# Performance work log

Measured on AMD Instinct MI355X. Metric: run time of the kernel, lower is better.

Reference implementation:

```python
import jax, jax.numpy as jnp
import numpy as np

HID = 64        # hid_size
NUM_LAYER = 3
NG = 16         # number of graphs in batch
NPG = 160       # nodes per graph
N = NG * NPG    # 2560 total nodes
DEG = 16
EPG = NPG * DEG # edges per graph
E = NG * EPG    # 40960 total edges
P = NG * NPG * NPG  # 409600 total (i,j) pairs from triu_indices(n, -n)
AV = 64         # atom feature vocab per column (9 columns)
BV = 8          # bond feature vocab per column (3 columns)
EPS = 1e-5


def setup_inputs() -> dict:
    rng = np.random.default_rng(0)
    key = jax.random.key(0)
    ks = jax.random.split(key, 16)

    # categorical node / edge features
    x = jnp.asarray(rng.integers(0, AV, size=(N, 9)), dtype=jnp.int32)
    edge_attr = jnp.asarray(rng.integers(0, BV, size=(E, 3)), dtype=jnp.int32)

    # within-graph random edges (sorted order not required for the math here)
    src_l = rng.integers(0, NPG, size=(NG, EPG))
    dst_l = rng.integers(0, NPG, size=(NG, EPG))
    gid = np.repeat(np.arange(NG), EPG)
    # flat position of edge (u,v) of graph g inside the concatenated all-pairs list
    epos = jnp.asarray(gid * NPG * NPG + src_l.reshape(-1) * NPG + dst_l.reshape(-1),
                       dtype=jnp.int32)

    # idx = concat([triu_indices(n, -n) + ptr[g]]) -> all pairs, row-major per graph
    g = np.arange(NG)[:, None, None]
    i = np.arange(NPG)[None, :, None]
    j = np.arange(NPG)[None, None, :]
    idx0 = jnp.asarray(np.broadcast_to(g * NPG + i, (NG, NPG, NPG)).reshape(-1).astype(np.int32))
    idx1 = jnp.asarray(np.broadcast_to(g * NPG + j, (NG, NPG, NPG)).reshape(-1).astype(np.int32))

    def lin(k, fan_in, fan_out):
        b = 1.0 / np.sqrt(fan_in)
        kw, kb = jax.random.split(k)
        return (jax.random.uniform(kw, (fan_in, fan_out), jnp.float32, -b, b),
                jax.random.uniform(kb, (fan_out,), jnp.float32, -b, b))

    atom_tables = jax.random.normal(ks[0], (9, AV, HID), jnp.float32) * 0.02
    bond_tables = jax.random.normal(ks[1], (3, BV, HID), jnp.float32) * 0.02
    W1, b1 = lin(ks[2], HID, HID)
    W2, b2 = lin(ks[3], HID, HID)
    We, be = lin(ks[4], HID, HID)
    L0_w, L0_b = lin(ks[5], 3 * HID, HID)
    L1_w, L1_b = lin(ks[6], HID, HID)
    L2_w, L2_b = lin(ks[7], HID, 1)
    g0 = jnp.ones((HID,), jnp.float32); beta0 = jnp.zeros((HID,), jnp.float32)
    g1 = jnp.ones((HID,), jnp.float32); beta1 = jnp.zeros((HID,), jnp.float32)

    return dict(atom_tables=atom_tables, bond_tables=bond_tables,
                W1=W1, b1=b1, W2=W2, b2=b2, We=We, be=be,
                L0_w=L0_w, L0_b=L0_b, L1_w=L1_w, L1_b=L1_b, L2_w=L2_w, L2_b=L2_b,
                g0=g0, beta0=beta0, g1=g1, beta1=beta1,
                x=x, edge_attr=edge_attr, idx0=idx0, idx1=idx1, epos=epos)


def _batchnorm(h, gamma, beta):
    mu = jnp.mean(h, axis=0)
    var = jnp.mean(jnp.square(h - mu), axis=0)  # biased var, torch training mode
    return (h - mu) * jax.lax.rsqrt(var + EPS) * gamma + beta


def reference(atom_tables, bond_tables, W1, b1, W2, b2, We, be,
              L0_w, L0_b, L1_w, L1_b, L2_w, L2_b,
              g0, beta0, g1, beta1,
              x, edge_attr, idx0, idx1, epos):
    # AtomEncoder / BondEncoder: sum of per-column embedding lookups
    cols9 = jnp.arange(9)[None, :]
    x_emb = atom_tables[cols9, x].sum(axis=1)          # [N, HID]
    cols3 = jnp.arange(3)[None, :]
    ea_emb = bond_tables[cols3, edge_attr].sum(axis=1)  # [E, HID]

    n1 = (x_emb @ W1 + b1)[idx0]                        # [P, HID]
    n2 = (x_emb @ W2 + b2)[idx1]                        # [P, HID]

    e = ea_emb @ We + be                                # [E, HID]
    # equivalent of SparseTensor.to_dense()[idx0, idx1] without the N^2 dense blowup;
    # duplicate edges sum, missing pairs are zero (matches to_dense semantics)
    e_pairs = jnp.zeros((P, HID), e.dtype).at[epos].add(e)

    emb = jnp.concatenate((n1, n2, e_pairs), axis=-1)   # [P, 3*HID]

    emb = jax.nn.relu(_batchnorm(emb @ L0_w + L0_b, g0, beta0))
    emb = jax.nn.relu(_batchnorm(emb @ L1_w + L1_b, g1, beta1))
    emb = emb @ L2_w + L2_b                             # [P, 1]
    return jnp.squeeze(emb, axis=-1)                    # [P]
```

## Files before the change

kernel.cpp:

```cpp
#include <hip/hip_runtime.h>
#include <hip/hip_bf16.h>

#define HID 64
#define NGr 16
#define NPG 160
#define NN  2560
#define EE  40960
#define PPG 25600
#define PT  409600
#define TT  25600
#define TPG 1600
#define AV  64
#define BV  8
#define EPSB 1e-5f

typedef __attribute__((ext_vector_type(8))) short short8v;
typedef __attribute__((ext_vector_type(4))) float f32x4;

static __device__ __forceinline__ unsigned short bf16_hi(float v) {
    return (unsigned short)(__float_as_uint(v) >> 16);
}
static __device__ __forceinline__ unsigned short bf16_rn(float v) {
    unsigned int u = __float_as_uint(v);
    u += 0x7FFFu + ((u >> 16) & 1u);
    return (unsigned short)(u >> 16);
}
static __device__ __forceinline__ float bf16_val(unsigned short h) {
    return __uint_as_float(((unsigned int)h) << 16);
}

__global__ void k_prep(const float* __restrict__ W1, const float* __restrict__ b1,
                       const float* __restrict__ W2, const float* __restrict__ b2,
                       const float* __restrict__ We, const float* __restrict__ be,
                       const float* __restrict__ L0w, const float* __restrict__ L0b,
                       const float* __restrict__ L1w,
                       float* __restrict__ W1c, float* __restrict__ W2c, float* __restrict__ Wec,
                       float* __restrict__ b1c, float* __restrict__ b2c, float* __restrict__ bec,
                       float* __restrict__ stats,
                       unsigned short* __restrict__ WBhi, unsigned short* __restrict__ WBlo) {
    int blk = blockIdx.x, tid = threadIdx.x;
    if (blk == 3) {
        stats[tid] = 0.f;
        for (int idx = tid; idx < 4096; idx += 256) {
            float w = L1w[idx];
            unsigned short hi = bf16_hi(w);
            float rem = w - bf16_val(hi);
            WBhi[idx] = hi;
            WBlo[idx] = bf16_hi(rem);
        }
        return;
    }
    const float* Wsrc = (blk == 0) ? W1 : (blk == 1) ? W2 : We;
    const float* bsrc = (blk == 0) ? b1 : (blk == 1) ? b2 : be;
    const float* L    = L0w + blk * 64 * 64;
    float* Wdst = (blk == 0) ? W1c : (blk == 1) ? W2c : Wec;
    float* bdst = (blk == 0) ? b1c : (blk == 1) ? b2c : bec;
    for (int idx = tid; idx < 4096; idx += 256) {
        int k = idx >> 6, h = idx & 63;
        float acc = 0.f;
        for (int m = 0; m < 64; ++m) acc = fmaf(Wsrc[k * 64 + m], L[m * 64 + h], acc);
        Wdst[idx] = acc;
    }
    if (tid < 64) {
        int h = tid;
        float acc = (blk == 0) ? L0b[h] : 0.f;
        for (int m = 0; m < 64; ++m) acc = fmaf(bsrc[m], L[m * 64 + h], acc);
        bdst[h] = acc;
    }
}

__global__ void __launch_bounds__(256) k_nodes(const float* __restrict__ atab, const int* __restrict__ x,
                        const float* __restrict__ W1c, const float* __restrict__ W2c,
                        const float* __restrict__ b1c, const float* __restrict__ b2c,
                        float* __restrict__ A, float* __restrict__ Bm) {
    int w = threadIdx.x >> 6, h = threadIdx.x & 63;
    int n = blockIdx.x * 4 + w;
    __shared__ float xe[4][64];
    float v = 0.f;
#pragma unroll
    for (int c = 0; c < 9; ++c) v += atab[c * AV * HID + x[n * 9 + c] * HID + h];
    xe[w][h] = v;
    float a = b1c[h], b = b2c[h];
#pragma unroll
    for (int k = 0; k < 64; ++k) {
        float xk = xe[w][k];
        a = fmaf(xk, W1c[k * 64 + h], a);
        b = fmaf(xk, W2c[k * 64 + h], b);
    }
    A[n * 64 + h] = a;
    Bm[n * 64 + h] = b;
}

__global__ void k_gstats(const float* __restrict__ A, const float* __restrict__ Bm,
                         float* __restrict__ stats) {
    int g = blockIdx.x;
    int h = threadIdx.x & 63, w = threadIdx.x >> 6;
    float sA = 0.f, sA2 = 0.f, sB = 0.f, sB2 = 0.f;
    for (int n = w; n < NPG; n += 4) {
        float a = A[(size_t)(g * NPG + n) * 64 + h];
        float b = Bm[(size_t)(g * NPG + n) * 64 + h];
        sA += a; sA2 = fmaf(a, a, sA2);
        sB += b; sB2 = fmaf(b, b, sB2);
    }
    __shared__ float ls[4][4][64];
    ls[w][0][h] = sA; ls[w][1][h] = sA2; ls[w][2][h] = sB; ls[w][3][h] = sB2;
    __syncthreads();
    if (w == 0) {
        sA  = ls[0][0][h] + ls[1][0][h] + ls[2][0][h] + ls[3][0][h];
        sA2 = ls[0][1][h] + ls[1][1][h] + ls[2][1][h] + ls[3][1][h];
        sB  = ls[0][2][h] + ls[1][2][h] + ls[2][2][h] + ls[3][2][h];
        sB2 = ls[0][3][h] + ls[1][3][h] + ls[2][3][h] + ls[3][3][h];
        atomicAdd(&stats[h], 160.f * (sA + sB));
        atomicAdd(&stats[64 + h], 160.f * (sA2 + sB2) + 2.f * sA * sB);
    }
}

__global__ void __launch_bounds__(256) k_edges(const float* __restrict__ btab, const int* __restrict__ eattr,
                                               const int* __restrict__ epos,
                                               const float* __restrict__ Wec, const float* __restrict__ bec,
                                               float* __restrict__ ewf, float* __restrict__ stats,
                                               int* __restrict__ bcount) {
    int h = threadIdx.x & 63;
    int el = threadIdx.x >> 6;
    __shared__ float ea[4][64];
    float ssum = 0.f;
    for (int base = blockIdx.x * 4; base < EE; base += gridDim.x * 4) {
        int e = base + el;
        float v = 0.f;
#pragma unroll
        for (int c = 0; c < 3; ++c) v += btab[c * BV * HID + eattr[e * 3 + c] * HID + h];
        ea[el][h] = v;
        float ew = bec[h];
#pragma unroll
        for (int k = 0; k < 64; ++k) ew = fmaf(ea[el][k], Wec[k * 64 + h], ew);
        ewf[(size_t)e * 64 + h] = ew;
        ssum += ew;
        if (h == 0) atomicAdd(&bcount[epos[e] >> 4], 1);
    }
    atomicAdd(&stats[h], ssum);
}

__global__ void k_scan(const int* __restrict__ bcount, int* __restrict__ boffs,
                       int* __restrict__ bcursor) {
    __shared__ int part[1024];
    int tid = threadIdx.x;
    int base = tid * (TT / 1024);
    int s = 0;
    for (int q = 0; q < TT / 1024; ++q) s += bcount[base + q];
    part[tid] = s;
    __syncthreads();
    for (int d = 1; d < 1024; d <<= 1) {
        int v = (tid >= d) ? part[tid - d] : 0;
        __syncthreads();
        part[tid] += v;
        __syncthreads();
    }
    int run = part[tid] - s;
    for (int q = 0; q < TT / 1024; ++q) {
        int c = bcount[base + q];
        boffs[base + q] = run;
        bcursor[base + q] = run;
        run += c;
    }
    if (tid == 1023) boffs[TT] = run;
}

__global__ void k_fill(const int* __restrict__ epos, int* __restrict__ bcursor,
                       int* __restrict__ elist) {
    int e = blockIdx.x * 256 + threadIdx.x;
    if (e >= EE) return;
    int p = epos[e];
    int t = p >> 4, jj = p & 15;
    int slot = atomicAdd(&bcursor[t], 1);
    elist[slot] = (e << 4) | jj;
}

__global__ void __launch_bounds__(256) k_scorr(const float* __restrict__ A, const float* __restrict__ Bm,
                                               const float* __restrict__ ewf,
                                               const int* __restrict__ boffs, const int* __restrict__ elist,
                                               float* __restrict__ stats) {
    __shared__ float run[4][16][64];
    int h = threadIdx.x & 63, w = threadIdx.x >> 6;
#pragma unroll
    for (int jj = 0; jj < 16; ++jj) run[w][jj][h] = 0.f;
    float ssacc = 0.f;
    int wave = blockIdx.x * 4 + w;
    int nw = gridDim.x * 4;
    for (int t = wave; t < TT; t += nw) {
        int be = boffs[t], en = boffs[t + 1];
        if (be == en) continue;
        int g = t / TPG;
        int rem = t - g * TPG;
        int i = rem / 10;
        int j0 = (rem - i * 10) << 4;
        float a = A[(size_t)(g * NPG + i) * 64 + h];
        for (int q = be; q < en; ++q) {
            int pk = elist[q];
            int e = pk >> 4, jj = pk & 15;
            float ew = ewf[(size_t)e * 64 + h];
            float base = a + Bm[(size_t)(g * NPG + j0 + jj) * 64 + h];
            float r = run[w][jj][h];
            ssacc += 2.f * (base + r) * ew + ew * ew;
            run[w][jj][h] = r + ew;
        }
        for (int q = be; q < en; ++q) run[w][elist[q] & 15][h] = 0.f;
    }
    atomicAdd(&stats[64 + h], ssacc);
}

__global__ void __launch_bounds__(256) k_main(const unsigned short* __restrict__ WBhi,
                                              const unsigned short* __restrict__ WBlo,
                                              const float* __restrict__ L1b,
                                              const float* __restrict__ g0, const float* __restrict__ beta0,
                                              const float* __restrict__ A, const float* __restrict__ Bm,
                                              const float* __restrict__ ewf,
                                              const int* __restrict__ boffs, const int* __restrict__ elist,
                                              uint2* __restrict__ zpk, float* __restrict__ stats) {
    int lane = threadIdx.x & 63;
    int wid  = blockIdx.x * 4 + (threadIdx.x >> 6);
    int nWaves = gridDim.x * 4;
    int r16 = lane & 15;
    int kg  = lane >> 4;

    const float invP = 1.f / (float)PT;
    float s0a[8], t0a[8], s0b[8], t0b[8];
#pragma unroll
    for (int j = 0; j < 8; ++j) {
        int k = kg * 8 + j;
        float mu = stats[k] * invP;
        float var = stats[64 + k] * invP - mu * mu;
        float inv = rsqrtf(var + EPSB);
        s0a[j] = g0[k] * inv;
        t0a[j] = fmaf(-mu, s0a[j], beta0[k]);
        int k2 = k + 32;
        float mu2 = stats[k2] * invP;
        float var2 = stats[64 + k2] * invP - mu2 * mu2;
        float inv2 = rsqrtf(var2 + EPSB);
        s0b[j] = g0[k2] * inv2;
        t0b[j] = fmaf(-mu2, s0b[j], beta0[k2]);
    }
    short8v Bhi[4][2], Blo[4][2];
#pragma unroll
    for (int ct = 0; ct < 4; ++ct)
#pragma unroll
        for (int ks = 0; ks < 2; ++ks)
#pragma unroll
            for (int j = 0; j < 8; ++j) {
                int k = ks * 32 + kg * 8 + j;
                int idx = k * 64 + ct * 16 + r16;
                Bhi[ct][ks][j] = (short)WBhi[idx];
                Blo[ct][ks][j] = (short)WBlo[idx];
            }
    float biasv[4];
#pragma unroll
    for (int ct = 0; ct < 4; ++ct) biasv[ct] = L1b[ct * 16 + r16];

    float sum[4] = {0.f, 0.f, 0.f, 0.f}, ssum[4] = {0.f, 0.f, 0.f, 0.f};

    for (int tile = wid; tile < TT; tile += nWaves) {
        int g = tile / TPG;
        int rem = tile - g * TPG;
        int i = rem / 10;
        int j0 = (rem - i * 10) << 4;
        const float* Ar = A + (size_t)(g * NPG + i) * 64;
        const float* Br = Bm + (size_t)(g * NPG + j0 + r16) * 64;
        float4 a0 = *reinterpret_cast<const float4*>(Ar + kg * 8);
        float4 a1 = *reinterpret_cast<const float4*>(Ar + kg * 8 + 4);
        float4 a2 = *reinterpret_cast<const float4*>(Ar + 32 + kg * 8);
        float4 a3 = *reinterpret_cast<const float4*>(Ar + 32 + kg * 8 + 4);
        float4 b0 = *reinterpret_cast<const float4*>(Br + kg * 8);
        float4 b1 = *reinterpret_cast<const float4*>(Br + kg * 8 + 4);
        float4 b2 = *reinterpret_cast<const float4*>(Br + 32 + kg * 8);
        float4 b3 = *reinterpret_cast<const float4*>(Br + 32 + kg * 8 + 4);
        float ha[8] = {a0.x + b0.x, a0.y + b0.y, a0.z + b0.z, a0.w + b0.w,
                       a1.x + b1.x, a1.y + b1.y, a1.z + b1.z, a1.w + b1.w};
        float hb[8] = {a2.x + b2.x, a2.y + b2.y, a2.z + b2.z, a2.w + b2.w,
                       a3.x + b3.x, a3.y + b3.y, a3.z + b3.z, a3.w + b3.w};
        int be = boffs[tile], en = boffs[tile + 1];
        for (int q = be; q < en; ++q) {
            int pk = elist[q];
            if (r16 == (pk & 15)) {
                const float* er = ewf + (size_t)(pk >> 4) * 64;
                float4 e0 = *reinterpret_cast<const float4*>(er + kg * 8);
                float4 e1 = *reinterpret_cast<const float4*>(er + kg * 8 + 4);
                float4 e2 = *reinterpret_cast<const float4*>(er + 32 + kg * 8);
                float4 e3 = *reinterpret_cast<const float4*>(er + 32 + kg * 8 + 4);
                ha[0] += e0.x; ha[1] += e0.y; ha[2] += e0.z; ha[3] += e0.w;
                ha[4] += e1.x; ha[5] += e1.y; ha[6] += e1.z; ha[7] += e1.w;
                hb[0] += e2.x; hb[1] += e2.y; hb[2] += e2.z; hb[3] += e2.w;
                hb[4] += e3.x; hb[5] += e3.y; hb[6] += e3.z; hb[7] += e3.w;
            }
        }
        short8v aHi0, aLo0, aHi1, aLo1;
#pragma unroll
        for (int j = 0; j < 8; ++j) {
            float hv = fmaxf(fmaf(ha[j], s0a[j], t0a[j]), 0.f);
            unsigned short hi = bf16_hi(hv);
            float remv = hv - bf16_val(hi);
            aHi0[j] = (short)hi;
            aLo0[j] = (short)bf16_hi(remv);
            float hv2 = fmaxf(fmaf(hb[j], s0b[j], t0b[j]), 0.f);
            unsigned short hi2 = bf16_hi(hv2);
            float rem2 = hv2 - bf16_val(hi2);
            aHi1[j] = (short)hi2;
            aLo1[j] = (short)bf16_hi(rem2);
        }
        f32x4 acc[4];
#pragma unroll
        for (int ct = 0; ct < 4; ++ct) acc[ct] = (f32x4){0.f, 0.f, 0.f, 0.f};
#pragma unroll
        for (int ct = 0; ct < 4; ++ct) {
            acc[ct] = __builtin_amdgcn_mfma_f32_16x16x32_bf16(aHi0, Bhi[ct][0], acc[ct], 0, 0, 0);
            acc[ct] = __builtin_amdgcn_mfma_f32_16x16x32_bf16(aHi0, Blo[ct][0], acc[ct], 0, 0, 0);
            acc[ct] = __builtin_amdgcn_mfma_f32_16x16x32_bf16(aLo0, Bhi[ct][0], acc[ct], 0, 0, 0);
            acc[ct] = __builtin_amdgcn_mfma_f32_16x16x32_bf16(aHi1, Bhi[ct][1], acc[ct], 0, 0, 0);
            acc[ct] = __builtin_amdgcn_mfma_f32_16x16x32_bf16(aHi1, Blo[ct][1], acc[ct], 0, 0, 0);
            acc[ct] = __builtin_amdgcn_mfma_f32_16x16x32_bf16(aLo1, Bhi[ct][1], acc[ct], 0, 0, 0);
        }
        uint2* tz = zpk + (size_t)tile * 256 + lane;
#pragma unroll
        for (int ct = 0; ct < 4; ++ct) {
            float z0 = acc[ct][0] + biasv[ct];
            float z1 = acc[ct][1] + biasv[ct];
            float z2 = acc[ct][2] + biasv[ct];
            float z3 = acc[ct][3] + biasv[ct];
            unsigned short u0 = bf16_rn(z0), u1 = bf16_rn(z1), u2 = bf16_rn(z2), u3 = bf16_rn(z3);
            float r0 = bf16_val(u0), r1 = bf16_val(u1), r2 = bf16_val(u2), r3 = bf16_val(u3);
            sum[ct] += (r0 + r1) + (r2 + r3);
            ssum[ct] += fmaf(r0, r0, fmaf(r1, r1, fmaf(r2, r2, r3 * r3)));
            uint2 pk;
            pk.x = (unsigned)u0 | ((unsigned)u1 << 16);
            pk.y = (unsigned)u2 | ((unsigned)u3 << 16);
            tz[ct * 64] = pk;
        }
    }
#pragma unroll
    for (int ct = 0; ct < 4; ++ct) {
        float s = sum[ct];
        s += __shfl_xor(s, 16);
        s += __shfl_xor(s, 32);
        float q = ssum[ct];
        q += __shfl_xor(q, 16);
        q += __shfl_xor(q, 32);
        if (kg == 0) {
            atomicAdd(&stats[128 + ct * 16 + r16], s);
            atomicAdd(&stats[192 + ct * 16 + r16], q);
        }
    }
}

__global__ void __launch_bounds__(256) k_final(const float* __restrict__ g1, const float* __restrict__ beta1,
                                               const float* __restrict__ L2w, const float* __restrict__ L2b,
                                               const uint2* __restrict__ zpk, float* __restrict__ out,
                                               const float* __restrict__ stats) {
    int lane = threadIdx.x & 63;
    int wid = blockIdx.x * 4 + (threadIdx.x >> 6);
    int nW = gridDim.x * 4;
    int r16 = lane & 15, kg = lane >> 4;
    const float invP = 1.f / (float)PT;
    float s1c[4], t1c[4], wv[4];
#pragma unroll
    for (int ct = 0; ct < 4; ++ct) {
        int col = ct * 16 + r16;
        float mu = stats[128 + col] * invP;
        float var = stats[192 + col] * invP - mu * mu;
        float inv = rsqrtf(var + EPSB);
        s1c[ct] = g1[col] * inv;
        t1c[ct] = fmaf(-mu, s1c[ct], beta1[col]);
        wv[ct] = L2w[col];
    }
    float obias = L2b[0];
    for (int tile = wid; tile < TT; tile += nW) {
        const uint2* tz = zpk + (size_t)tile * 256 + lane;
        uint2 cc[4] = {tz[0], tz[64], tz[128], tz[192]};
        float p0 = 0.f, p1 = 0.f, p2 = 0.f, p3 = 0.f;
#pragma unroll
        for (int ct = 0; ct < 4; ++ct) {
            float z0 = bf16_val((unsigned short)(cc[ct].x & 0xffffu));
            float z1 = bf16_val((unsigned short)(cc[ct].x >> 16));
            float z2 = bf16_val((unsigned short)(cc[ct].y & 0xffffu));
            float z3 = bf16_val((unsigned short)(cc[ct].y >> 16));
            p0 = fmaf(fmaxf(fmaf(z0, s1c[ct], t1c[ct]), 0.f), wv[ct], p0);
            p1 = fmaf(fmaxf(fmaf(z1, s1c[ct], t1c[ct]), 0.f), wv[ct], p1);
            p2 = fmaf(fmaxf(fmaf(z2, s1c[ct], t1c[ct]), 0.f), wv[ct], p2);
            p3 = fmaf(fmaxf(fmaf(z3, s1c[ct], t1c[ct]), 0.f), wv[ct], p3);
        }
#pragma unroll
        for (int d = 1; d < 16; d <<= 1) {
            p0 += __shfl_xor(p0, d);
            p1 += __shfl_xor(p1, d);
            p2 += __shfl_xor(p2, d);
            p3 += __shfl_xor(p3, d);
        }
        if (r16 == 0) {
            float4 o = {p0 + obias, p1 + obias, p2 + obias, p3 + obias};
            *reinterpret_cast<float4*>(out + tile * 16 + kg * 4) = o;
        }
    }
}

extern "C" void kernel_launch(void* const* d_in, const int* in_sizes, int n_in,
                              void* d_out, int out_size, void* d_ws, size_t ws_size,
                              hipStream_t stream) {
    const float* atab  = (const float*)d_in[0];
    const float* btab  = (const float*)d_in[1];
    const float* W1    = (const float*)d_in[2];
    const float* b1    = (const float*)d_in[3];
    const float* W2    = (const float*)d_in[4];
    const float* b2    = (const float*)d_in[5];
    const float* We    = (const float*)d_in[6];
    const float* be    = (const float*)d_in[7];
    const float* L0w   = (const float*)d_in[8];
    const float* L0b   = (const float*)d_in[9];
    const float* L1w   = (const float*)d_in[10];
    const float* L1b   = (const float*)d_in[11];
    const float* L2w   = (const float*)d_in[12];
    const float* L2b   = (const float*)d_in[13];
    const float* g0    = (const float*)d_in[14];
    const float* beta0 = (const float*)d_in[15];
    const float* g1    = (const float*)d_in[16];
    const float* beta1 = (const float*)d_in[17];
    const int*   x     = (const int*)d_in[18];
    const int*   eattr = (const int*)d_in[19];
    const int*   epos  = (const int*)d_in[22];
    float* out = (float*)d_out;

    float* ws = (float*)d_ws;
    float* zpk_f = ws;
    float* A    = zpk_f + 13107200;
    float* Bm   = A + (size_t)NN * 64;
    float* ewf  = Bm + (size_t)NN * 64;
    float* W1c  = ewf + (size_t)EE * 64;
    float* W2c  = W1c + 4096;
    float* Wec  = W2c + 4096;
    float* b1c  = Wec + 4096;
    float* b2c  = b1c + 64;
    float* bec  = b2c + 64;
    float* stats = bec + 64;
    unsigned short* WBhi = (unsigned short*)(stats + 256);
    unsigned short* WBlo = WBhi + 4096;
    int* bcount  = (int*)(WBlo + 4096);
    int* boffs   = bcount + TT;
    int* bcursor = boffs + TT + 1;
    int* elist   = bcursor + TT;

    uint2* zpk = (uint2*)zpk_f;

    hipMemsetAsync(bcount, 0, TT * sizeof(int), stream);

    k_prep<<<4, 256, 0, stream>>>(W1, b1, W2, b2, We, be, L0w, L0b, L1w,
                                  W1c, W2c, Wec, b1c, b2c, bec, stats, WBhi, WBlo);
    k_nodes<<<NN / 4, 256, 0, stream>>>(atab, x, W1c, W2c, b1c, b2c, A, Bm);
    k_gstats<<<NGr, 256, 0, stream>>>(A, Bm, stats);
    k_edges<<<512, 256, 0, stream>>>(btab, eattr, epos, Wec, bec, ewf, stats, bcount);
    k_scan<<<1, 1024, 0, stream>>>(bcount, boffs, bcursor);
    k_fill<<<EE / 256, 256, 0, stream>>>(epos, bcursor, elist);
    k_scorr<<<256, 256, 0, stream>>>(A, Bm, ewf, boffs, elist, stats);
    k_main<<<512, 256, 0, stream>>>(WBhi, WBlo, L1b, g0, beta0, A, Bm, ewf, boffs, elist,
                                    zpk, stats);
    k_final<<<1024, 256, 0, stream>>>(g1, beta1, L2w, L2b, zpk, out, stats);
}
```

Measured before the change: 283.8 us.

## Split stats correction, parallelize scan, vectorize z stores, widen final grid

```diff
diff --git a/kernel.cpp b/kernel.cpp
--- a/kernel.cpp
+++ b/kernel.cpp
@@ -118,12 +118,13 @@
 __global__ void __launch_bounds__(256) k_edges(const float* __restrict__ btab, const int* __restrict__ eattr,
                                                const int* __restrict__ epos,
                                                const float* __restrict__ Wec, const float* __restrict__ bec,
+                                               const float* __restrict__ A, const float* __restrict__ Bm,
                                                float* __restrict__ ewf, float* __restrict__ stats,
                                                int* __restrict__ bcount) {
     int h = threadIdx.x & 63;
     int el = threadIdx.x >> 6;
     __shared__ float ea[4][64];
-    float ssum = 0.f;
+    float ssum = 0.f, ss2 = 0.f;
     for (int base = blockIdx.x * 4; base < EE; base += gridDim.x * 4) {
         int e = base + el;
         float v = 0.f;
@@ -134,35 +135,58 @@
 #pragma unroll
         for (int k = 0; k < 64; ++k) ew = fmaf(ea[el][k], Wec[k * 64 + h], ew);
         ewf[(size_t)e * 64 + h] = ew;
+        int p = epos[e];
+        int gg = p / PPG;
+        int rp = p - gg * PPG;
+        int ii = rp / NPG;
+        int jj = rp - ii * NPG;
+        float D = A[(size_t)(gg * NPG + ii) * 64 + h] + Bm[(size_t)(gg * NPG + jj) * 64 + h];
         ssum += ew;
-        if (h == 0) atomicAdd(&bcount[epos[e] >> 4], 1);
+        ss2 += (2.f * D + ew) * ew;
+        if (h == 0) atomicAdd(&bcount[p >> 4], 1);
     }
     atomicAdd(&stats[h], ssum);
-}
-
-__global__ void k_scan(const int* __restrict__ bcount, int* __restrict__ boffs,
-                       int* __restrict__ bcursor) {
-    __shared__ int part[1024];
+    atomicAdd(&stats[64 + h], ss2);
+}
+
+__global__ void k_scan1(const int* __restrict__ bcount, int* __restrict__ boffs,
+                        int* __restrict__ bsum) {
+    __shared__ int sh[256];
     int tid = threadIdx.x;
-    int base = tid * (TT / 1024);
-    int s = 0;
-    for (int q = 0; q < TT / 1024; ++q) s += bcount[base + q];
-    part[tid] = s;
+    int t = blockIdx.x * 256 + tid;
+    int v = bcount[t];
+    sh[tid] = v;
     __syncthreads();
-    for (int d = 1; d < 1024; d <<= 1) {
-        int v = (tid >= d) ? part[tid - d] : 0;
+    for (int d = 1; d < 256; d <<= 1) {
+        int u = (tid >= d) ? sh[tid - d] : 0;
         __syncthreads();
-        part[tid] += v;
+        sh[tid] += u;
         __syncthreads();
     }
-    int run = part[tid] - s;
-    for (int q = 0; q < TT / 1024; ++q) {
-        int c = bcount[base + q];
-        boffs[base + q] = run;
-        bcursor[base + q] = run;
-        run += c;
-    }
-    if (tid == 1023) boffs[TT] = run;
+    boffs[t] = sh[tid] - v;
+    if (tid == 255) bsum[blockIdx.x] = sh[255];
+}
+__global__ void k_scan2(int* __restrict__ bsum) {
+    __shared__ int sh[256];
+    int tid = threadIdx.x;
+    int v = (tid < 100) ? bsum[tid] : 0;
+    sh[tid] = v;
+    __syncthreads();
+    for (int d = 1; d < 256; d <<= 1) {
+        int u = (tid >= d) ? sh[tid - d] : 0;
+        __syncthreads();
+        sh[tid] += u;
+        __syncthreads();
+    }
+    if (tid < 100) bsum[tid] = sh[tid] - v;
+}
+__global__ void k_scan3(const int* __restrict__ bcount, const int* __restrict__ bsum,
+                        int* __restrict__ boffs, int* __restrict__ bcursor) {
+    int t = blockIdx.x * 256 + threadIdx.x;
+    int o = boffs[t] + bsum[blockIdx.x];
+    boffs[t] = o;
+    bcursor[t] = o;
+    if (t == TT - 1) boffs[TT] = o + bcount[t];
 }
 
 __global__ void k_fill(const int* __restrict__ epos, int* __restrict__ bcursor,
@@ -175,37 +199,30 @@
     elist[slot] = (e << 4) | jj;
 }
 
-__global__ void __launch_bounds__(256) k_scorr(const float* __restrict__ A, const float* __restrict__ Bm,
-                                               const float* __restrict__ ewf,
+__global__ void __launch_bounds__(256) k_cross(const float* __restrict__ ewf,
                                                const int* __restrict__ boffs, const int* __restrict__ elist,
                                                float* __restrict__ stats) {
-    __shared__ float run[4][16][64];
     int h = threadIdx.x & 63, w = threadIdx.x >> 6;
-#pragma unroll
-    for (int jj = 0; jj < 16; ++jj) run[w][jj][h] = 0.f;
-    float ssacc = 0.f;
-    int wave = blockIdx.x * 4 + w;
-    int nw = gridDim.x * 4;
-    for (int t = wave; t < TT; t += nw) {
+    float acc = 0.f;
+    for (int t = blockIdx.x * 4 + w; t < TT; t += gridDim.x * 4) {
         int be = boffs[t], en = boffs[t + 1];
-        if (be == en) continue;
-        int g = t / TPG;
-        int rem = t - g * TPG;
-        int i = rem / 10;
-        int j0 = (rem - i * 10) << 4;
-        float a = A[(size_t)(g * NPG + i) * 64 + h];
-        for (int q = be; q < en; ++q) {
-            int pk = elist[q];
-            int e = pk >> 4, jj = pk & 15;
-            float ew = ewf[(size_t)e * 64 + h];
-            float base = a + Bm[(size_t)(g * NPG + j0 + jj) * 64 + h];
-            float r = run[w][jj][h];
-            ssacc += 2.f * (base + r) * ew + ew * ew;
-            run[w][jj][h] = r + ew;
-        }
-        for (int q = be; q < en; ++q) run[w][elist[q] & 15][h] = 0.f;
-    }
-    atomicAdd(&stats[64 + h], ssacc);
+        if (en - be < 2) continue;
+        for (int q1 = be; q1 < en; ++q1) {
+            int pk1 = elist[q1];
+            float e1 = ewf[(size_t)(pk1 >> 4) * 64 + h];
+            for (int q2 = q1 + 1; q2 < en; ++q2) {
+                int pk2 = elist[q2];
+                if ((pk1 & 15) == (pk2 & 15))
+                    acc += 2.f * e1 * ewf[(size_t)(pk2 >> 4) * 64 + h];
+            }
+        }
+    }
+    __shared__ float ls[64];
+    if (threadIdx.x < 64) ls[threadIdx.x] = 0.f;
+    __syncthreads();
+    atomicAdd(&ls[h], acc);
+    __syncthreads();
+    if (threadIdx.x < 64) atomicAdd(&stats[64 + threadIdx.x], ls[threadIdx.x]);
 }
 
 __global__ void __launch_bounds__(256) k_main(const unsigned short* __restrict__ WBhi,
@@ -317,7 +334,7 @@
             acc[ct] = __builtin_amdgcn_mfma_f32_16x16x32_bf16(aHi1, Blo[ct][1], acc[ct], 0, 0, 0);
             acc[ct] = __builtin_amdgcn_mfma_f32_16x16x32_bf16(aLo1, Bhi[ct][1], acc[ct], 0, 0, 0);
         }
-        uint2* tz = zpk + (size_t)tile * 256 + lane;
+        unsigned upk[8];
 #pragma unroll
         for (int ct = 0; ct < 4; ++ct) {
             float z0 = acc[ct][0] + biasv[ct];
@@ -328,11 +345,12 @@
             float r0 = bf16_val(u0), r1 = bf16_val(u1), r2 = bf16_val(u2), r3 = bf16_val(u3);
             sum[ct] += (r0 + r1) + (r2 + r3);
             ssum[ct] += fmaf(r0, r0, fmaf(r1, r1, fmaf(r2, r2, r3 * r3)));
-            uint2 pk;
-            pk.x = (unsigned)u0 | ((unsigned)u1 << 16);
-            pk.y = (unsigned)u2 | ((unsigned)u3 << 16);
-            tz[ct * 64] = pk;
-        }
+            upk[ct * 2]     = (unsigned)u0 | ((unsigned)u1 << 16);
+            upk[ct * 2 + 1] = (unsigned)u2 | ((unsigned)u3 << 16);
+        }
+        uint4* t4 = reinterpret_cast<uint4*>(zpk + (size_t)tile * 256 + lane * 4);
+        t4[0] = (uint4){upk[0], upk[1], upk[2], upk[3]};
+        t4[1] = (uint4){upk[4], upk[5], upk[6], upk[7]};
     }
 #pragma unroll
     for (int ct = 0; ct < 4; ++ct) {
@@ -371,15 +389,16 @@
     }
     float obias = L2b[0];
     for (int tile = wid; tile < TT; tile += nW) {
-        const uint2* tz = zpk + (size_t)tile * 256 + lane;
-        uint2 cc[4] = {tz[0], tz[64], tz[128], tz[192]};
+        const uint4* t4 = reinterpret_cast<const uint4*>(zpk + (size_t)tile * 256 + lane * 4);
+        uint4 w0 = t4[0], w1 = t4[1];
+        unsigned cc[8] = {w0.x, w0.y, w0.z, w0.w, w1.x, w1.y, w1.z, w1.w};
         float p0 = 0.f, p1 = 0.f, p2 = 0.f, p3 = 0.f;
 #pragma unroll
         for (int ct = 0; ct < 4; ++ct) {
-            float z0 = bf16_val((unsigned short)(cc[ct].x & 0xffffu));
-            float z1 = bf16_val((unsigned short)(cc[ct].x >> 16));
-            float z2 = bf16_val((unsigned short)(cc[ct].y & 0xffffu));
-            float z3 = bf16_val((unsigned short)(cc[ct].y >> 16));
+            float z0 = bf16_val((unsigned short)(cc[ct * 2] & 0xffffu));
+            float z1 = bf16_val((unsigned short)(cc[ct * 2] >> 16));
+            float z2 = bf16_val((unsigned short)(cc[ct * 2 + 1] & 0xffffu));
+            float z3 = bf16_val((unsigned short)(cc[ct * 2 + 1] >> 16));
             p0 = fmaf(fmaxf(fmaf(z0, s1c[ct], t1c[ct]), 0.f), wv[ct], p0);
             p1 = fmaf(fmaxf(fmaf(z1, s1c[ct], t1c[ct]), 0.f), wv[ct], p1);
             p2 = fmaf(fmaxf(fmaf(z2, s1c[ct], t1c[ct]), 0.f), wv[ct], p2);
@@ -443,6 +462,7 @@
     int* boffs   = bcount + TT;
     int* bcursor = boffs + TT + 1;
     int* elist   = bcursor + TT;
+    int* bsum    = elist + EE;
 
     uint2* zpk = (uint2*)zpk_f;
 
@@ -452,11 +472,13 @@
                                   W1c, W2c, Wec, b1c, b2c, bec, stats, WBhi, WBlo);
     k_nodes<<<NN / 4, 256, 0, stream>>>(atab, x, W1c, W2c, b1c, b2c, A, Bm);
     k_gstats<<<NGr, 256, 0, stream>>>(A, Bm, stats);
-    k_edges<<<512, 256, 0, stream>>>(btab, eattr, epos, Wec, bec, ewf, stats, bcount);
-    k_scan<<<1, 1024, 0, stream>>>(bcount, boffs, bcursor);
+    k_edges<<<512, 256, 0, stream>>>(btab, eattr, epos, Wec, bec, A, Bm, ewf, stats, bcount);
+    k_scan1<<<TT / 256, 256, 0, stream>>>(bcount, boffs, bsum);
+    k_scan2<<<1, 256, 0, stream>>>(bsum);
+    k_scan3<<<TT / 256, 256, 0, stream>>>(bcount, bsum, boffs, bcursor);
     k_fill<<<EE / 256, 256, 0, stream>>>(epos, bcursor, elist);
-    k_scorr<<<256, 256, 0, stream>>>(A, Bm, ewf, boffs, elist, stats);
+    k_cross<<<256, 256, 0, stream>>>(ewf, boffs, elist, stats);
     k_main<<<512, 256, 0, stream>>>(WBhi, WBlo, L1b, g0, beta0, A, Bm, ewf, boffs, elist,
                                     zpk, stats);
-    k_final<<<1024, 256, 0, stream>>>(g1, beta1, L2w, L2b, zpk, out, stats);
-}
+    k_final<<<4096, 256, 0, stream>>>(g1, beta1, L2w, L2b, zpk, out, stats);
+}
```

Result: faster. 257.7 us (-9.2%).
